# Performance work log

Measured on AMD Instinct MI355X. Metric: run time of the kernel, lower is better.

## Reference

```python
import jax, jax.numpy as jnp
import numpy as np

N_NODES = 100000
N_EDGES = 1600000
IN_DIM = 128
HID_DIM = 128
OUT_DIM = 64


def gcn_conv(x, W, b, edge_index):
    """GCNConv with add_self_loops, symmetric degree norm, add-aggregation.

    Math matches PyG: out[i] = sum_{(j,i) in E+selfloops} norm_ji * (x_j @ W) + b
    Since lin is linear and there is no edge_attr, we transform x once before
    the gather instead of per-edge (identical result, far less FLOPs/traffic).
    """
    n = x.shape[0]
    loop = jnp.arange(n, dtype=edge_index.dtype)
    row = jnp.concatenate([edge_index[0], loop])  # source nodes (x_j)
    col = jnp.concatenate([edge_index[1], loop])  # destination nodes
    # degree over destinations (includes self loops -> deg >= 1, no div by 0)
    deg = jax.ops.segment_sum(jnp.ones_like(col, dtype=x.dtype), col, num_segments=n)
    dinv = jax.lax.rsqrt(deg)
    norm = dinv[row] * dinv[col]  # [E+N]
    h = x @ W  # [N, out] transform once
    msg = norm[:, None] * h[row]  # [E+N, out] gathered per-edge messages
    out = jax.ops.segment_sum(msg, col, num_segments=n)  # scatter-add
    return out + b


def setup_inputs() -> dict:
    key = jax.random.key(0)
    k1, k2, k3, k4 = jax.random.split(key, 4)
    x = jax.random.normal(k1, (N_NODES, IN_DIM), dtype=jnp.float32)
    edge_index = jax.random.randint(k2, (2, N_EDGES), 0, N_NODES, dtype=jnp.int64)
    # glorot-ish init
    W1 = jax.random.normal(k3, (IN_DIM, HID_DIM), dtype=jnp.float32) * (2.0 / (IN_DIM + HID_DIM)) ** 0.5
    W2 = jax.random.normal(k4, (HID_DIM, OUT_DIM), dtype=jnp.float32) * (2.0 / (HID_DIM + OUT_DIM)) ** 0.5
    b1 = jnp.zeros((HID_DIM,), dtype=jnp.float32)
    b2 = jnp.zeros((OUT_DIM,), dtype=jnp.float32)
    return {"x": x, "edge_index": edge_index, "W1": W1, "b1": b1, "W2": W2, "b2": b2}


def reference(x, edge_index, W1, b1, W2, b2):
    # GCN.forward with prompt_type=None, pooling=False, eval mode (dropout is identity)
    h = gcn_conv(x, W1, b1, edge_index)
    h = jax.nn.relu(h)
    out = gcn_conv(h, W2, b2, edge_index)
    return out
```

## Files before the change

### kernel.cpp

```cpp
#include <hip/hip_runtime.h>


#define DIN 128
#define DHID 128
#define DOUT 64
#define ELLW 64
#define GPART 8
#define BPG 512

typedef __attribute__((ext_vector_type(4))) float f32x4;
typedef __attribute__((ext_vector_type(8))) short bf16x8;

__device__ __forceinline__ float bf2f(unsigned int u16) {
    return __uint_as_float(u16 << 16);
}
__device__ __forceinline__ unsigned short f2bf(float f) {
    unsigned int u = __float_as_uint(f);
    u += 0x7fffu + ((u >> 16) & 1u);
    return (unsigned short)(u >> 16);
}
__device__ __forceinline__ unsigned int pack2(float a, float b) {
    return (unsigned int)f2bf(a) | ((unsigned int)f2bf(b) << 16);
}

__global__ __launch_bounds__(256) void k_packW(const float* __restrict__ W1,
                                               const float* __restrict__ W2,
                                               unsigned short* __restrict__ w1p,
                                               unsigned short* __restrict__ w2p,
                                               int* __restrict__ deg, int N) {
    int id = blockIdx.x * 256 + threadIdx.x;
    if (id < 2048) {
        int lane = id & 63, s = (id >> 6) & 3, t = id >> 8;
        int n = t * 16 + (lane & 15);
        int k0 = s * 32 + (lane >> 4) * 8;
#pragma unroll
        for (int j = 0; j < 8; ++j)
            w1p[(size_t)id * 8 + j] = f2bf(W1[(k0 + j) * DHID + n]);
    } else if (id < 3072) {
        int id2 = id - 2048;
        int lane = id2 & 63, s = (id2 >> 6) & 3, t = id2 >> 8;
        int n = t * 16 + (lane & 15);
        int k0 = s * 32 + (lane >> 4) * 8;
#pragma unroll
        for (int j = 0; j < 8; ++j)
            w2p[(size_t)id2 * 8 + j] = f2bf(W2[(k0 + j) * DOUT + n]);
    }
    for (int i = id; i < N; i += 12 * 256) deg[i] = 0;
}

__device__ __forceinline__ void fill_edge(int c, int r, int lo, int hi,
                                          int* __restrict__ deg, int* __restrict__ ell) {
    if (c >= lo && c < hi) {
        int k = atomicAdd(&deg[c], 1);
        if (k < ELLW) ell[(size_t)c * ELLW + k] = r;
    }
}

__global__ __launch_bounds__(256) void k_fill_gemm1(
        const int* __restrict__ rows, const int* __restrict__ cols,
        int* __restrict__ deg, int* __restrict__ ell,
        int E, int perBlock, int R, int GOCT, int GB,
        const float* __restrict__ x, const unsigned short* __restrict__ w1p,
        unsigned short* __restrict__ h1b, int N) {
    int bid = (int)blockIdx.x;
    int o = bid >> 3;
    int lane7 = bid & 7;
    int m = o / 3;
    int p = o - 3 * m;
    if (p == 2 && m < GOCT) {
        int gemmIdx = m * 8 + lane7;
        if (gemmIdx >= GB) return;
        int wave = threadIdx.x >> 6, lane = threadIdx.x & 63;
        int quad = lane >> 4, qr = lane & 15;
        int rowBase = gemmIdx * 64 + wave * 16;
        int arow = rowBase + qr;
        bool rowOK = arow < N;
        f32x4 acc[8] = {};
#pragma unroll
        for (int s = 0; s < 4; ++s) {
            bf16x8 a = {};
            if (rowOK) {
                const float* ap = x + (size_t)arow * DIN + s * 32 + quad * 8;
                float4 lo = *(const float4*)ap;
                float4 hi = *(const float4*)(ap + 4);
                a[0] = (short)f2bf(lo.x); a[1] = (short)f2bf(lo.y);
                a[2] = (short)f2bf(lo.z); a[3] = (short)f2bf(lo.w);
                a[4] = (short)f2bf(hi.x); a[5] = (short)f2bf(hi.y);
                a[6] = (short)f2bf(hi.z); a[7] = (short)f2bf(hi.w);
            }
#pragma unroll
            for (int t = 0; t < 8; ++t) {
                bf16x8 b = *(const bf16x8*)(w1p + ((size_t)(t * 4 + s) * 64 + lane) * 8);
                acc[t] = __builtin_amdgcn_mfma_f32_16x16x32_bf16(a, b, acc[t], 0, 0, 0);
            }
        }
#pragma unroll
        for (int t = 0; t < 8; ++t)
#pragma unroll
            for (int i = 0; i < 4; ++i) {
                int r = rowBase + quad * 4 + i;
                if (r < N) h1b[(size_t)r * DHID + t * 16 + qr] = f2bf(acc[t][i]);
            }
        return;
    }
    int gemBefore = (m < GOCT) ? m : GOCT;
    int chunk = o - gemBefore;
    int g = lane7;
    int lo = g * R, hi = lo + R;
    int eBeg = chunk * perBlock;
    int eEnd = eBeg + perBlock; if (eEnd > E) eEnd = E;
    for (int e = eBeg + 4 * threadIdx.x; e < eEnd; e += 4 * 256) {
        if (e + 3 < eEnd) {
            int4 c4 = *(const int4*)(cols + e);
            int4 r4 = *(const int4*)(rows + e);
            fill_edge(c4.x, r4.x, lo, hi, deg, ell);
            fill_edge(c4.y, r4.y, lo, hi, deg, ell);
            fill_edge(c4.z, r4.z, lo, hi, deg, ell);
            fill_edge(c4.w, r4.w, lo, hi, deg, ell);
        } else {
            for (int j = e; j < eEnd; ++j) fill_edge(cols[j], rows[j], lo, hi, deg, ell);
        }
    }
}

__global__ __launch_bounds__(256) void k_gather1(const int* __restrict__ deg,
                                                 const int* __restrict__ ell,
                                                 const uint2* __restrict__ h1v,
                                                 const float* __restrict__ b1,
                                                 uint2* __restrict__ hactv, int N) {
    int w = (blockIdx.x * 256 + threadIdx.x) >> 6;
    int lane = threadIdx.x & 63;
    if (w >= N) return;
    int d = deg[w]; if (d > ELLW) d = ELLW;
    int iv0 = ell[(size_t)w * ELLW + lane];
    int iv = (lane < d) ? iv0 : 0;
    float dv = (lane < d) ? rsqrtf((float)(deg[iv] + 1)) : 0.f;
    int half = lane >> 5, col = lane & 31;
    float a0 = 0.f, a1 = 0.f, a2 = 0.f, a3 = 0.f;
    int e = 0;
    for (; e + 16 <= d; e += 16) {
        int s[8]; float wg[8]; uint2 v[8];
#pragma unroll
        for (int j = 0; j < 8; ++j) {
            int idx = e + 2 * j + half;
            s[j] = __shfl(iv, idx); wg[j] = __shfl(dv, idx);
        }
#pragma unroll
        for (int j = 0; j < 8; ++j) v[j] = h1v[(size_t)s[j] * 32 + col];
#pragma unroll
        for (int j = 0; j < 8; ++j) {
            a0 = fmaf(wg[j], bf2f(v[j].x & 0xffffu), a0);
            a1 = fmaf(wg[j], bf2f(v[j].x >> 16), a1);
            a2 = fmaf(wg[j], bf2f(v[j].y & 0xffffu), a2);
            a3 = fmaf(wg[j], bf2f(v[j].y >> 16), a3);
        }
    }
    for (; e + 8 <= d; e += 8) {
        int s[4]; float wg[4]; uint2 v[4];
#pragma unroll
        for (int j = 0; j < 4; ++j) {
            int idx = e + 2 * j + half;
            s[j] = __shfl(iv, idx); wg[j] = __shfl(dv, idx);
        }
#pragma unroll
        for (int j = 0; j < 4; ++j) v[j] = h1v[(size_t)s[j] * 32 + col];
#pragma unroll
        for (int j = 0; j < 4; ++j) {
            a0 = fmaf(wg[j], bf2f(v[j].x & 0xffffu), a0);
            a1 = fmaf(wg[j], bf2f(v[j].x >> 16), a1);
            a2 = fmaf(wg[j], bf2f(v[j].y & 0xffffu), a2);
            a3 = fmaf(wg[j], bf2f(v[j].y >> 16), a3);
        }
    }
    for (; e < d; e += 2) {
        int idx = e + half;
        int s0 = __shfl(iv, idx); float w0 = __shfl(dv, idx);
        uint2 v0 = h1v[(size_t)s0 * 32 + col];
        a0 = fmaf(w0, bf2f(v0.x & 0xffffu), a0);
        a1 = fmaf(w0, bf2f(v0.x >> 16), a1);
        a2 = fmaf(w0, bf2f(v0.y & 0xffffu), a2);
        a3 = fmaf(w0, bf2f(v0.y >> 16), a3);
    }
    a0 += __shfl_xor(a0, 32); a1 += __shfl_xor(a1, 32);
    a2 += __shfl_xor(a2, 32); a3 += __shfl_xor(a3, 32);
    float di = rsqrtf((float)(d + 1)), self = di * di;
    uint2 hv = h1v[(size_t)w * 32 + col];
    float4 bv = *(const float4*)(b1 + 4 * col);
    float r0 = fmaf(di, a0, fmaf(self, bf2f(hv.x & 0xffffu), bv.x));
    float r1 = fmaf(di, a1, fmaf(self, bf2f(hv.x >> 16), bv.y));
    float r2 = fmaf(di, a2, fmaf(self, bf2f(hv.y & 0xffffu), bv.z));
    float r3 = fmaf(di, a3, fmaf(self, bf2f(hv.y >> 16), bv.w));
    if (lane < 32) {
        uint2 ov;
        ov.x = pack2(fmaxf(r0, 0.f), fmaxf(r1, 0.f));
        ov.y = pack2(fmaxf(r2, 0.f), fmaxf(r3, 0.f));
        hactv[(size_t)w * 32 + col] = ov;
    }
}

__global__ __launch_bounds__(256) void k_gemm2(const unsigned short* __restrict__ hactb,
                                               const unsigned short* __restrict__ w2p,
                                               unsigned short* __restrict__ h2b, int N) {
    int wave = threadIdx.x >> 6, lane = threadIdx.x & 63;
    int quad = lane >> 4, qr = lane & 15;
    int rowBase = blockIdx.x * 64 + wave * 16;
    int arow = rowBase + qr;
    bool rowOK = arow < N;
    f32x4 acc[4] = {};
#pragma unroll
    for (int s = 0; s < 4; ++s) {
        bf16x8 a = {};
        if (rowOK) a = *(const bf16x8*)(hactb + (size_t)arow * DHID + s * 32 + quad * 8);
#pragma unroll
        for (int t = 0; t < 4; ++t) {
            bf16x8 b = *(const bf16x8*)(w2p + ((size_t)(t * 4 + s) * 64 + lane) * 8);
            acc[t] = __builtin_amdgcn_mfma_f32_16x16x32_bf16(a, b, acc[t], 0, 0, 0);
        }
    }
#pragma unroll
    for (int t = 0; t < 4; ++t)
#pragma unroll
        for (int i = 0; i < 4; ++i) {
            int r = rowBase + quad * 4 + i;
            if (r < N) h2b[(size_t)r * DOUT + t * 16 + qr] = f2bf(acc[t][i]);
        }
}

__global__ __launch_bounds__(256) void k_gather2(const int* __restrict__ deg,
                                                 const int* __restrict__ ell,
                                                 const unsigned int* __restrict__ h2v,
                                                 const float* __restrict__ b2,
                                                 float* __restrict__ out, int N) {
    int w = (blockIdx.x * 256 + threadIdx.x) >> 6;
    int lane = threadIdx.x & 63;
    if (w >= N) return;
    int d = deg[w]; if (d > ELLW) d = ELLW;
    int iv0 = ell[(size_t)w * ELLW + lane];
    int iv = (lane < d) ? iv0 : 0;
    float dv = (lane < d) ? rsqrtf((float)(deg[iv] + 1)) : 0.f;
    int half = lane >> 5, col = lane & 31;
    float a0 = 0.f, a1 = 0.f;
    int e = 0;
    for (; e + 16 <= d; e += 16) {
        int s[8]; float wg[8]; unsigned int v[8];
#pragma unroll
        for (int j = 0; j < 8; ++j) {
            int idx = e + 2 * j + half;
            s[j] = __shfl(iv, idx); wg[j] = __shfl(dv, idx);
        }
#pragma unroll
        for (int j = 0; j < 8; ++j) v[j] = h2v[(size_t)s[j] * 32 + col];
#pragma unroll
        for (int j = 0; j < 8; ++j) {
            a0 = fmaf(wg[j], bf2f(v[j] & 0xffffu), a0);
            a1 = fmaf(wg[j], bf2f(v[j] >> 16), a1);
        }
    }
    for (; e + 8 <= d; e += 8) {
        int s[4]; float wg[4]; unsigned int v[4];
#pragma unroll
        for (int j = 0; j < 4; ++j) {
            int idx = e + 2 * j + half;
            s[j] = __shfl(iv, idx); wg[j] = __shfl(dv, idx);
        }
#pragma unroll
        for (int j = 0; j < 4; ++j) v[j] = h2v[(size_t)s[j] * 32 + col];
#pragma unroll
        for (int j = 0; j < 4; ++j) {
            a0 = fmaf(wg[j], bf2f(v[j] & 0xffffu), a0);
            a1 = fmaf(wg[j], bf2f(v[j] >> 16), a1);
        }
    }
    for (; e < d; e += 2) {
        int idx = e + half;
        int s0 = __shfl(iv, idx); float w0 = __shfl(dv, idx);
        unsigned int v0 = h2v[(size_t)s0 * 32 + col];
        a0 = fmaf(w0, bf2f(v0 & 0xffffu), a0);
        a1 = fmaf(w0, bf2f(v0 >> 16), a1);
    }
    a0 += __shfl_xor(a0, 32); a1 += __shfl_xor(a1, 32);
    float di = rsqrtf((float)(d + 1)), self = di * di;
    unsigned int hv = h2v[(size_t)w * 32 + col];
    float2 bv = *(const float2*)(b2 + 2 * col);
    float r0 = fmaf(di, a0, fmaf(self, bf2f(hv & 0xffffu), bv.x));
    float r1 = fmaf(di, a1, fmaf(self, bf2f(hv >> 16), bv.y));
    if (lane < 32) {
        float2 ov; ov.x = r0; ov.y = r1;
        *(float2*)(out + (size_t)w * DOUT + 2 * col) = ov;
    }
}

extern "C" void kernel_launch(void* const* d_in, const int* in_sizes, int n_in,
                              void* d_out, int out_size, void* d_ws, size_t ws_size,
                              hipStream_t stream) {
    const float* x  = (const float*)d_in[0];
    const int*   ei = (const int*)d_in[1];
    const float* W1 = (const float*)d_in[2];
    const float* b1 = (const float*)d_in[3];
    const float* W2 = (const float*)d_in[4];
    const float* b2 = (const float*)d_in[5];

    const int N = in_sizes[0] / DIN;
    const int E = in_sizes[1] / 2;
    const int* rows = ei;
    const int* cols = ei + E;

    char* p = (char*)d_ws;
    int*   ell  = (int*)p;                    p += (size_t)N * ELLW * 4;
    unsigned short* h1b = (unsigned short*)p;   p += (size_t)N * DHID * 2;
    unsigned short* hactb = (unsigned short*)p; p += (size_t)N * DHID * 2;
    unsigned short* w1p = (unsigned short*)p;   p += (size_t)2048 * 8 * 2;
    unsigned short* w2p = (unsigned short*)p;   p += (size_t)1024 * 8 * 2;
    int*   deg  = (int*)p;                    p += (size_t)N * 4;
    unsigned short* h2b = h1b;

    const int R = (N + GPART - 1) / GPART;
    int perBlock = (E + BPG - 1) / BPG;
    perBlock = (perBlock + 3) & ~3;
    const int GB = (N + 63) / 64;
    const int GOCT = (GB + 7) / 8;
    const int OCT = BPG + GOCT;

    k_packW<<<12, 256, 0, stream>>>(W1, W2, w1p, w2p, deg, N);

    k_fill_gemm1<<<8 * OCT, 256, 0, stream>>>(rows, cols, deg, ell, E, perBlock, R,
                                              GOCT, GB, x, w1p, h1b, N);

    k_gather1<<<(N + 3) / 4, 256, 0, stream>>>(deg, ell, (const uint2*)h1b,
                                               b1, (uint2*)hactb, N);

    k_gemm2<<<(N + 63) / 64, 256, 0, stream>>>(hactb, w2p, h2b, N);
    k_gather2<<<(N + 3) / 4, 256, 0, stream>>>(deg, ell, (const unsigned int*)h2b,
                                               b2, (float*)d_out, N);
}
```

Baseline: 302.7 us.

## Fuse first-layer aggregation with second-layer GEMM through LDS staging

Merges the layer-1 gather/ReLU kernel with the layer-2 MFMA GEMM. Each 256-thread block now aggregates 64 nodes, 16 per wave processed serially, and writes the activated bf16 rows to a shared-memory tile. After a barrier the block runs the MFMA product on that tile. This removes the global write and re-read of the full hidden activation matrix and one kernel launch. In exchange there are far fewer blocks, and each wave loops serially over its nodes, which may reduce latency hiding for the irregular gathers.

```diff
diff --git a/kernel.cpp b/kernel.cpp
--- a/kernel.cpp
+++ b/kernel.cpp
@@ -123,94 +123,92 @@
     }
 }
 
-__global__ __launch_bounds__(256) void k_gather1(const int* __restrict__ deg,
-                                                 const int* __restrict__ ell,
-                                                 const uint2* __restrict__ h1v,
-                                                 const float* __restrict__ b1,
-                                                 uint2* __restrict__ hactv, int N) {
-    int w = (blockIdx.x * 256 + threadIdx.x) >> 6;
+__global__ __launch_bounds__(256) void k_gather1g2(const int* __restrict__ deg,
+                                                   const int* __restrict__ ell,
+                                                   const uint2* __restrict__ h1v,
+                                                   const float* __restrict__ b1,
+                                                   const unsigned short* __restrict__ w2p,
+                                                   unsigned short* __restrict__ h2b, int N) {
+    __shared__ unsigned short hact_s[64][136];
+    int wv = threadIdx.x >> 6;
     int lane = threadIdx.x & 63;
-    if (w >= N) return;
-    int d = deg[w]; if (d > ELLW) d = ELLW;
-    int iv0 = ell[(size_t)w * ELLW + lane];
-    int iv = (lane < d) ? iv0 : 0;
-    float dv = (lane < d) ? rsqrtf((float)(deg[iv] + 1)) : 0.f;
     int half = lane >> 5, col = lane & 31;
-    float a0 = 0.f, a1 = 0.f, a2 = 0.f, a3 = 0.f;
-    int e = 0;
-    for (; e + 16 <= d; e += 16) {
-        int s[8]; float wg[8]; uint2 v[8];
-#pragma unroll
-        for (int j = 0; j < 8; ++j) {
-            int idx = e + 2 * j + half;
-            s[j] = __shfl(iv, idx); wg[j] = __shfl(dv, idx);
-        }
-#pragma unroll
-        for (int j = 0; j < 8; ++j) v[j] = h1v[(size_t)s[j] * 32 + col];
-#pragma unroll
-        for (int j = 0; j < 8; ++j) {
-            a0 = fmaf(wg[j], bf2f(v[j].x & 0xffffu), a0);
-            a1 = fmaf(wg[j], bf2f(v[j].x >> 16), a1);
-            a2 = fmaf(wg[j], bf2f(v[j].y & 0xffffu), a2);
-            a3 = fmaf(wg[j], bf2f(v[j].y >> 16), a3);
-        }
-    }
-    for (; e + 8 <= d; e += 8) {
-        int s[4]; float wg[4]; uint2 v[4];
-#pragma unroll
-        for (int j = 0; j < 4; ++j) {
-            int idx = e + 2 * j + half;
-            s[j] = __shfl(iv, idx); wg[j] = __shfl(dv, idx);
-        }
-#pragma unroll
-        for (int j = 0; j < 4; ++j) v[j] = h1v[(size_t)s[j] * 32 + col];
-#pragma unroll
-        for (int j = 0; j < 4; ++j) {
-            a0 = fmaf(wg[j], bf2f(v[j].x & 0xffffu), a0);
-            a1 = fmaf(wg[j], bf2f(v[j].x >> 16), a1);
-            a2 = fmaf(wg[j], bf2f(v[j].y & 0xffffu), a2);
-            a3 = fmaf(wg[j], bf2f(v[j].y >> 16), a3);
-        }
-    }
-    for (; e < d; e += 2) {
-        int idx = e + half;
-        int s0 = __shfl(iv, idx); float w0 = __shfl(dv, idx);
-        uint2 v0 = h1v[(size_t)s0 * 32 + col];
-        a0 = fmaf(w0, bf2f(v0.x & 0xffffu), a0);
-        a1 = fmaf(w0, bf2f(v0.x >> 16), a1);
-        a2 = fmaf(w0, bf2f(v0.y & 0xffffu), a2);
-        a3 = fmaf(w0, bf2f(v0.y >> 16), a3);
-    }
-    a0 += __shfl_xor(a0, 32); a1 += __shfl_xor(a1, 32);
-    a2 += __shfl_xor(a2, 32); a3 += __shfl_xor(a3, 32);
-    float di = rsqrtf((float)(d + 1)), self = di * di;
-    uint2 hv = h1v[(size_t)w * 32 + col];
+    int base = blockIdx.x * 64;
     float4 bv = *(const float4*)(b1 + 4 * col);
-    float r0 = fmaf(di, a0, fmaf(self, bf2f(hv.x & 0xffffu), bv.x));
-    float r1 = fmaf(di, a1, fmaf(self, bf2f(hv.x >> 16), bv.y));
-    float r2 = fmaf(di, a2, fmaf(self, bf2f(hv.y & 0xffffu), bv.z));
-    float r3 = fmaf(di, a3, fmaf(self, bf2f(hv.y >> 16), bv.w));
-    if (lane < 32) {
-        uint2 ov;
-        ov.x = pack2(fmaxf(r0, 0.f), fmaxf(r1, 0.f));
-        ov.y = pack2(fmaxf(r2, 0.f), fmaxf(r3, 0.f));
-        hactv[(size_t)w * 32 + col] = ov;
-    }
-}
-
-__global__ __launch_bounds__(256) void k_gemm2(const unsigned short* __restrict__ hactb,
-                                               const unsigned short* __restrict__ w2p,
-                                               unsigned short* __restrict__ h2b, int N) {
-    int wave = threadIdx.x >> 6, lane = threadIdx.x & 63;
+    for (int i = 0; i < 16; ++i) {
+        int w = base + wv * 16 + i;
+        if (w >= N) break;
+        int d = deg[w]; if (d > ELLW) d = ELLW;
+        int iv0 = ell[(size_t)w * ELLW + lane];
+        int iv = (lane < d) ? iv0 : 0;
+        float dv = (lane < d) ? rsqrtf((float)(deg[iv] + 1)) : 0.f;
+        float a0 = 0.f, a1 = 0.f, a2 = 0.f, a3 = 0.f;
+        int e = 0;
+        for (; e + 16 <= d; e += 16) {
+            int s[8]; float wg[8]; uint2 v[8];
+#pragma unroll
+            for (int j = 0; j < 8; ++j) {
+                int idx = e + 2 * j + half;
+                s[j] = __shfl(iv, idx); wg[j] = __shfl(dv, idx);
+            }
+#pragma unroll
+            for (int j = 0; j < 8; ++j) v[j] = h1v[(size_t)s[j] * 32 + col];
+#pragma unroll
+            for (int j = 0; j < 8; ++j) {
+                a0 = fmaf(wg[j], bf2f(v[j].x & 0xffffu), a0);
+                a1 = fmaf(wg[j], bf2f(v[j].x >> 16), a1);
+                a2 = fmaf(wg[j], bf2f(v[j].y & 0xffffu), a2);
+                a3 = fmaf(wg[j], bf2f(v[j].y >> 16), a3);
+            }
+        }
+        for (; e + 8 <= d; e += 8) {
+            int s[4]; float wg[4]; uint2 v[4];
+#pragma unroll
+            for (int j = 0; j < 4; ++j) {
+                int idx = e + 2 * j + half;
+                s[j] = __shfl(iv, idx); wg[j] = __shfl(dv, idx);
+            }
+#pragma unroll
+            for (int j = 0; j < 4; ++j) v[j] = h1v[(size_t)s[j] * 32 + col];
+#pragma unroll
+            for (int j = 0; j < 4; ++j) {
+                a0 = fmaf(wg[j], bf2f(v[j].x & 0xffffu), a0);
+                a1 = fmaf(wg[j], bf2f(v[j].x >> 16), a1);
+                a2 = fmaf(wg[j], bf2f(v[j].y & 0xffffu), a2);
+                a3 = fmaf(wg[j], bf2f(v[j].y >> 16), a3);
+            }
+        }
+        for (; e < d; e += 2) {
+            int idx = e + half;
+            int s0 = __shfl(iv, idx); float w0 = __shfl(dv, idx);
+            uint2 v0 = h1v[(size_t)s0 * 32 + col];
+            a0 = fmaf(w0, bf2f(v0.x & 0xffffu), a0);
+            a1 = fmaf(w0, bf2f(v0.x >> 16), a1);
+            a2 = fmaf(w0, bf2f(v0.y & 0xffffu), a2);
+            a3 = fmaf(w0, bf2f(v0.y >> 16), a3);
+        }
+        a0 += __shfl_xor(a0, 32); a1 += __shfl_xor(a1, 32);
+        a2 += __shfl_xor(a2, 32); a3 += __shfl_xor(a3, 32);
+        float di = rsqrtf((float)(d + 1)), self = di * di;
+        uint2 hv = h1v[(size_t)w * 32 + col];
+        float r0 = fmaf(di, a0, fmaf(self, bf2f(hv.x & 0xffffu), bv.x));
+        float r1 = fmaf(di, a1, fmaf(self, bf2f(hv.x >> 16), bv.y));
+        float r2 = fmaf(di, a2, fmaf(self, bf2f(hv.y & 0xffffu), bv.z));
+        float r3 = fmaf(di, a3, fmaf(self, bf2f(hv.y >> 16), bv.w));
+        if (lane < 32) {
+            uint2 ov;
+            ov.x = pack2(fmaxf(r0, 0.f), fmaxf(r1, 0.f));
+            ov.y = pack2(fmaxf(r2, 0.f), fmaxf(r3, 0.f));
+            *(uint2*)&hact_s[wv * 16 + i][4 * col] = ov;
+        }
+    }
+    __syncthreads();
     int quad = lane >> 4, qr = lane & 15;
-    int rowBase = blockIdx.x * 64 + wave * 16;
-    int arow = rowBase + qr;
-    bool rowOK = arow < N;
+    int arow = wv * 16 + qr;
     f32x4 acc[4] = {};
 #pragma unroll
     for (int s = 0; s < 4; ++s) {
-        bf16x8 a = {};
-        if (rowOK) a = *(const bf16x8*)(hactb + (size_t)arow * DHID + s * 32 + quad * 8);
+        bf16x8 a = *(const bf16x8*)&hact_s[arow][s * 32 + quad * 8];
 #pragma unroll
         for (int t = 0; t < 4; ++t) {
             bf16x8 b = *(const bf16x8*)(w2p + ((size_t)(t * 4 + s) * 64 + lane) * 8);
@@ -221,7 +219,7 @@
     for (int t = 0; t < 4; ++t)
 #pragma unroll
         for (int i = 0; i < 4; ++i) {
-            int r = rowBase + quad * 4 + i;
+            int r = base + wv * 16 + quad * 4 + i;
             if (r < N) h2b[(size_t)r * DOUT + t * 16 + qr] = f2bf(acc[t][i]);
         }
 }
@@ -308,11 +306,10 @@
     char* p = (char*)d_ws;
     int*   ell  = (int*)p;                    p += (size_t)N * ELLW * 4;
     unsigned short* h1b = (unsigned short*)p;   p += (size_t)N * DHID * 2;
-    unsigned short* hactb = (unsigned short*)p; p += (size_t)N * DHID * 2;
+    unsigned short* h2b = (unsigned short*)p;   p += (size_t)N * DOUT * 2;
     unsigned short* w1p = (unsigned short*)p;   p += (size_t)2048 * 8 * 2;
     unsigned short* w2p = (unsigned short*)p;   p += (size_t)1024 * 8 * 2;
     int*   deg  = (int*)p;                    p += (size_t)N * 4;
-    unsigned short* h2b = h1b;
 
     const int R = (N + GPART - 1) / GPART;
     int perBlock = (E + BPG - 1) / BPG;
@@ -326,10 +323,9 @@
     k_fill_gemm1<<<8 * OCT, 256, 0, stream>>>(rows, cols, deg, ell, E, perBlock, R,
                                               GOCT, GB, x, w1p, h1b, N);
 
-    k_gather1<<<(N + 3) / 4, 256, 0, stream>>>(deg, ell, (const uint2*)h1b,
-                                               b1, (uint2*)hactb, N);
-
-    k_gemm2<<<(N + 63) / 64, 256, 0, stream>>>(hactb, w2p, h2b, N);
+    k_gather1g2<<<(N + 63) / 64, 256, 0, stream>>>(deg, ell, (const uint2*)h1b,
+                                                   b1, w2p, h2b, N);
+
     k_gather2<<<(N + 3) / 4, 256, 0, stream>>>(deg, ell, (const unsigned int*)h2b,
                                                b2, (float*)d_out, N);
 }
```

After: 322.6 us. +6.6%, slower.
